# Performance work log

Measured on AMD Instinct MI355X. Metric: run time of the kernel, lower is better.

## Reference

```python
import jax, jax.numpy as jnp
import numpy as np

B, S, D, H = 8, 1024, 1024, 16
DK = D // H


def setup_inputs() -> dict:
    key = jax.random.key(0)
    ks = jax.random.split(key, 12)
    sc = 1.0 / np.sqrt(D)
    return {
        "query": jax.random.normal(ks[0], (B, S, D), jnp.float32),
        "key": jax.random.normal(ks[1], (B, S, D), jnp.float32),
        "value": jax.random.normal(ks[2], (B, S, D), jnp.float32),
        "Wq": jax.random.normal(ks[3], (D, D), jnp.float32) * sc,
        "bq": jnp.zeros((D,), jnp.float32),
        "Wk": jax.random.normal(ks[4], (D, D), jnp.float32) * sc,
        "bk": jnp.zeros((D,), jnp.float32),
        "Wv": jax.random.normal(ks[5], (D, D), jnp.float32) * sc,
        "bv": jnp.zeros((D,), jnp.float32),
        "Wa": jax.random.normal(ks[6], (D, D), jnp.float32) * sc,
        "ba": jnp.zeros((D,), jnp.float32),
        "qvec": jax.random.normal(ks[7], (D,), jnp.float32),
    }


def reference(query, key, value, Wq, bq, Wk, bk, Wv, bv, Wa, ba, qvec):
    # project and split heads: [B,S,D] -> [B,H,S,DK]
    def split(x, W, b):
        y = x @ W.T + b
        return y.reshape(B, S, H, DK).transpose(0, 2, 1, 3)

    q = split(query, Wq, bq)
    k = split(key, Wk, bk)
    v = split(value, Wv, bv)

    scores = jnp.einsum('bhqd,bhkd->bhqk', q, k) / jnp.sqrt(jnp.float32(DK))
    p = jax.nn.softmax(scores, axis=-1)          # dropout p=0 -> identity
    x = jnp.einsum('bhqk,bhkd->bhqd', p, v)
    x = x.transpose(0, 2, 1, 3).reshape(B, S, D)  # [B,S,D]

    # attention2 pooling head
    a = jnp.tanh(x @ Wa.T + ba) @ qvec           # [B,S]
    alpha = jax.nn.softmax(a, axis=-1)
    return jnp.einsum('bs,bsd->bd', alpha, x)    # [B,D]
```

## Files before the change

### kernel.cpp

```cpp
#include <hip/hip_runtime.h>

typedef __bf16 bf16;
typedef __attribute__((ext_vector_type(8))) __bf16 bf16x8;
typedef __attribute__((ext_vector_type(4))) __bf16 bf16x4;
typedef __attribute__((ext_vector_type(4))) float f32x4;

#define GLDS16(g, l) __builtin_amdgcn_global_load_lds( \
    (const __attribute__((address_space(1))) void*)(g), \
    (__attribute__((address_space(3))) void*)(l), 16, 0, 0)

#define MFMA16(a, b, c) __builtin_amdgcn_mfma_f32_16x16x32_bf16(a, b, c, 0, 0, 0)

#define TR16(dst, addr, off) \
  asm volatile("ds_read_b64_tr_b16 %0, %1 offset:" #off : "=v"(dst) : "v"(addr))

struct CvtAll { const float* in[7]; bf16* out[7]; };

__global__ __launch_bounds__(256) void f2b_all(CvtAll a) {
  const int i = blockIdx.x * 256 + threadIdx.x;
  const float* in;
  bf16* out;
  int off;
  if (blockIdx.y < 3) {
    in = a.in[blockIdx.y];
    out = a.out[blockIdx.y];
    off = i;
  } else {
    if (i >= 524288) return;
    const int widx = 3 + (i >> 17);
    in = a.in[widx];
    out = a.out[widx];
    off = i & 131071;
  }
  const f32x4* p = (const f32x4*)in + (size_t)off * 2;
  f32x4 x = p[0], y = p[1];
  bf16x8 o;
  o[0] = (bf16)x[0]; o[1] = (bf16)x[1]; o[2] = (bf16)x[2]; o[3] = (bf16)x[3];
  o[4] = (bf16)y[0]; o[5] = (bf16)y[1]; o[6] = (bf16)y[2]; o[7] = (bf16)y[3];
  ((bf16x8*)out)[off] = o;
}

template <int EPI, int MF>
__device__ __forceinline__ void gemm_body8(
    const bf16* __restrict__ A, const bf16* __restrict__ Bw,
    const float* __restrict__ bias, const float* __restrict__ qv,
    bf16* __restrict__ C, float* __restrict__ part,
    const int row0, const int col0, const int N, const int K) {
  constexpr int BM = MF * 32;
  constexpr int ASZ = MF * 1024;
  constexpr int BUF = 2 * ASZ + 16384;
  constexpr int RSH = (MF == 8) ? 8 : 7;
  __shared__ __attribute__((aligned(16))) bf16 L[2 * BUF];
  const int tid = threadIdx.x;
  const int wid = tid >> 6, lane = tid & 63;
  const int g = lane >> 4, lc = lane & 15;
  const int wr = wid >> 2, wc = wid & 3;

  const bf16* gA = A + (size_t)(row0 + (tid & (BM - 1))) * K + (tid >> RSH) * 8;
  const bf16* gB = Bw + (size_t)(col0 + (tid & 255)) * K + (tid >> 8) * 8;
  const int d0 = (tid - lane) * 8;

#define STG_A(T, kh) do { \
    const bf16* gp_ = gA + (T) * 64 + (kh) * 32; \
    bf16* lp_ = L + ((T) & 1) * BUF + (kh) * ASZ + d0; \
    GLDS16(gp_, lp_); \
    if constexpr (MF == 8) GLDS16(gp_ + 16, lp_ + 4096); } while (0)
#define STG_B(T, kh) do { \
    const bf16* gp_ = gB + (T) * 64 + (kh) * 32; \
    bf16* lp_ = L + ((T) & 1) * BUF + 2 * ASZ + (kh) * 8192 + d0; \
    GLDS16(gp_, lp_); GLDS16(gp_ + 16, lp_ + 4096); } while (0)
#define RD_A(c, kh) do { \
    _Pragma("unroll") for (int m_ = 0; m_ < MF; ++m_) \
      af[m_] = *(const bf16x8*)&L[(c) * BUF + (kh) * ASZ + g * (BM * 8) + \
                                  (wr * (MF * 16) + m_ * 16 + lc) * 8]; \
  } while (0)
#define RD_B(c, kh, nh) do { \
    bf[0] = *(const bf16x8*)&L[(c) * BUF + 2 * ASZ + (kh) * 8192 + g * 2048 + \
                               (wc * 64 + (nh) * 32 + lc) * 8]; \
    bf[1] = *(const bf16x8*)&L[(c) * BUF + 2 * ASZ + (kh) * 8192 + g * 2048 + \
                               (wc * 64 + (nh) * 32 + 16 + lc) * 8]; \
  } while (0)
#define BARS \
    __builtin_amdgcn_s_barrier(); \
    asm volatile("s_waitcnt lgkmcnt(0)" ::: "memory"); \
    __builtin_amdgcn_sched_barrier(0);
#define MM(nh) do { \
    __builtin_amdgcn_s_setprio(1); \
    _Pragma("unroll") for (int m_ = 0; m_ < MF; ++m_) { \
      acc[m_][(nh) * 2 + 0] = MFMA16(af[m_], bf[0], acc[m_][(nh) * 2 + 0]); \
      acc[m_][(nh) * 2 + 1] = MFMA16(af[m_], bf[1], acc[m_][(nh) * 2 + 1]); \
    } \
    __builtin_amdgcn_s_setprio(0); } while (0)
#define ENDP do { \
    __builtin_amdgcn_s_barrier(); \
    asm volatile("" ::: "memory"); \
    __builtin_amdgcn_sched_barrier(0); } while (0)
#define VGATE() do { \
    if constexpr (MF == 8) { asm volatile("s_waitcnt vmcnt(6)" ::: "memory"); } \
    else                   { asm volatile("s_waitcnt vmcnt(4)" ::: "memory"); } } while (0)

  const f32x4 z4 = {0.f, 0.f, 0.f, 0.f};
  f32x4 acc[MF][4];
#pragma unroll
  for (int m = 0; m < MF; ++m)
#pragma unroll
    for (int n = 0; n < 4; ++n) acc[m][n] = z4;

  bf16x8 af[MF], bf[2];
  const int NT = K >> 6;
  const int NI = NT >> 1;

  STG_A(0, 0); STG_B(0, 0); STG_A(0, 1); STG_B(0, 1);
  STG_A(1, 0); STG_B(1, 0); STG_A(1, 1);
  VGATE();
  ENDP;

  for (int i = 0; i < NI; ++i) {
    const int t1 = 2 * i + 1, t2 = 2 * i + 2, t3 = 2 * i + 3;
    const bool p2 = t2 < NT, p3 = t3 < NT;
    RD_A(0, 0); RD_B(0, 0, 0);
    STG_B(t1, 1);
    BARS; MM(0); ENDP;
    RD_B(0, 0, 1);
    if (p2) STG_A(t2, 0);
    BARS; MM(1); ENDP;
    RD_A(0, 1); RD_B(0, 1, 0);
    if (p2) STG_B(t2, 0);
    BARS; MM(0); ENDP;
    RD_B(0, 1, 1);
    if (p2) STG_A(t2, 1);
    BARS; MM(1);
    if (p2) { VGATE(); }
    else    { asm volatile("s_waitcnt vmcnt(0)" ::: "memory"); }
    ENDP;
    RD_A(1, 0); RD_B(1, 0, 0);
    if (p2) STG_B(t2, 1);
    BARS; MM(0); ENDP;
    RD_B(1, 0, 1);
    if (p3) STG_A(t3, 0);
    BARS; MM(1); ENDP;
    RD_A(1, 1); RD_B(1, 1, 0);
    if (p3) STG_B(t3, 0);
    BARS; MM(0); ENDP;
    RD_B(1, 1, 1);
    if (p3) STG_A(t3, 1);
    BARS; MM(1);
    VGATE();
    ENDP;
  }

#undef STG_A
#undef STG_B
#undef RD_A
#undef RD_B
#undef BARS
#undef MM
#undef ENDP
#undef VGATE

  if constexpr (EPI == 0) {
#pragma unroll
    for (int n = 0; n < 4; ++n) {
      const int col = col0 + wc * 64 + n * 16 + lc;
      const float bb = bias[col];
#pragma unroll
      for (int m = 0; m < MF; ++m)
#pragma unroll
        for (int r = 0; r < 4; ++r) {
          const int row = row0 + wr * (MF * 16) + m * 16 + g * 4 + r;
          C[(size_t)row * N + col] = (bf16)(acc[m][n][r] + bb);
        }
    }
  } else {
    float ps[MF][4];
#pragma unroll
    for (int m = 0; m < MF; ++m)
#pragma unroll
      for (int r = 0; r < 4; ++r) ps[m][r] = 0.f;
#pragma unroll
    for (int n = 0; n < 4; ++n) {
      const int col = col0 + wc * 64 + n * 16 + lc;
      const float bb = bias[col];
      const float qq = qv[col];
#pragma unroll
      for (int m = 0; m < MF; ++m)
#pragma unroll
        for (int r = 0; r < 4; ++r)
          ps[m][r] += tanhf(acc[m][n][r] + bb) * qq;
    }
    float* pdst = part + (size_t)((col0 >> 8) * 4 + wc) * 8192;
#pragma unroll
    for (int m = 0; m < MF; ++m)
#pragma unroll
      for (int r = 0; r < 4; ++r) {
        float v = ps[m][r];
        v += __shfl_xor(v, 1); v += __shfl_xor(v, 2);
        v += __shfl_xor(v, 4); v += __shfl_xor(v, 8);
        if (lc == 0) {
          const int row = row0 + wr * (MF * 16) + m * 16 + g * 4 + r;
          pdst[row] = v;
        }
      }
  }
}

__device__ __forceinline__ void swz128(int phys, int& row0, int& col0) {
  const int lg = (phys & 7) * 16 + (phys >> 3);
  row0 = (lg >> 2) * 256;
  col0 = (lg & 3) * 256;
}

__device__ __forceinline__ void swz256(int phys, int& row0, int& col0) {
  const int lg = (phys & 7) * 32 + (phys >> 3);
  row0 = (lg >> 2) * 128;
  col0 = (lg & 3) * 256;
}

struct GemmSet { const bf16* A; const bf16* Bw; const float* bias; bf16* C; };
struct Gemm3Args { GemmSet s[3]; };

__global__ __launch_bounds__(512, 2) void gemm3_kernel(Gemm3Args a) {
  const GemmSet s = a.s[blockIdx.y];
  int row0, col0;
  swz128(blockIdx.x, row0, col0);
  gemm_body8<0, 8>(s.A, s.Bw, s.bias, nullptr, s.C, nullptr, row0, col0, 1024, 1024);
}

__global__ __launch_bounds__(512, 2) void gemm_a_kernel(
    const bf16* __restrict__ A, const bf16* __restrict__ Bw,
    const float* __restrict__ bias, const float* __restrict__ qv,
    float* __restrict__ part) {
  int row0, col0;
  swz256(blockIdx.x, row0, col0);
  gemm_body8<1, 4>(A, Bw, bias, qv, nullptr, part, row0, col0, 1024, 1024);
}

__global__ __launch_bounds__(256) void attn_kernel(
    const bf16* __restrict__ qp, const bf16* __restrict__ kp,
    const bf16* __restrict__ vp, bf16* __restrict__ xb, float* __restrict__ xf) {
  constexpr int S = 1024, D = 1024;
  __shared__ __attribute__((aligned(16))) bf16 Ks[8192];
  __shared__ __attribute__((aligned(16))) bf16 Vs[8192];
  __shared__ __attribute__((aligned(16))) bf16 Ps[4096];
  const int tid = threadIdx.x, wid = tid >> 6, lane = tid & 63;
  const int g = lane >> 4, lc = lane & 15;
  const int b = blockIdx.x >> 4, h = blockIdx.x & 15;
  const int q0 = blockIdx.y * 64;
  const size_t base = (size_t)b * S * D + (size_t)h * 64;

  bf16x8 qf[2];
  {
    const bf16* qrow = qp + base + (size_t)(q0 + wid * 16 + lc) * D;
    qf[0] = *(const bf16x8*)(qrow + g * 8);
    qf[1] = *(const bf16x8*)(qrow + 32 + g * 8);
#pragma unroll
    for (int j = 0; j < 8; ++j) {
      qf[0][j] = (bf16)((float)qf[0][j] * 0.125f);
      qf[1][j] = (bf16)((float)qf[1][j] * 0.125f);
    }
  }
  float m_s = -1e30f, l_s = 0.f;
  const f32x4 z4 = {0.f, 0.f, 0.f, 0.f};
  f32x4 ax[4];
#pragma unroll
  for (int m = 0; m < 4; ++m) ax[m] = z4;

  const int c0 = tid, c1 = tid + 256;
  const bf16* gK0 = kp + base + (size_t)(c0 & 63) * D + (c0 >> 6) * 8;
  const bf16* gK1 = kp + base + (size_t)(c1 & 63) * D + (c1 >> 6) * 8;
  bf16* lK0 = Ks + (size_t)(c0 - lane) * 8;
  bf16* lK1 = Ks + (size_t)(c1 - lane) * 8;
  const bf16* gV0 = vp + base + (size_t)((c0 >> 5) * 4 + ((c0 >> 1) & 3)) * D +
                    ((c0 >> 3) & 3) * 16 + (c0 & 1) * 8;
  const bf16* gV1 = vp + base + (size_t)((c1 >> 5) * 4 + ((c1 >> 1) & 3)) * D +
                    ((c1 >> 3) & 3) * 16 + (c1 & 1) * 8;
  bf16* lV0 = Vs + (size_t)(c0 - lane) * 8;
  bf16* lV1 = Vs + (size_t)(c1 - lane) * 8;

  bf16* pw = Ps + wid * 1024;
  const int pswz_a = lc & 3, pswz_b = (lc >> 2) & 3;
  const unsigned vaddr0 =
      (unsigned)(uintptr_t)(const __attribute__((address_space(3))) bf16*)(Vs + 512 * g + 4 * lc);

  GLDS16(gK0, lK0);
  GLDS16(gK1, lK1);
  GLDS16(gV0, lV0);
  GLDS16(gV1, lV1);

  for (int t = 0; t < 16; ++t) {
    __syncthreads();
    const int cur = t & 1;
    if (t < 15) {
      const size_t off = (size_t)(t + 1) * 64 * D;
      const int nb = cur ^ 1;
      GLDS16(gK0 + off, lK0 + nb * 4096);
      GLDS16(gK1 + off, lK1 + nb * 4096);
      GLDS16(gV0 + off, lV0 + nb * 4096);
      GLDS16(gV1 + off, lV1 + nb * 4096);
    }
    const bf16* Kb = Ks + cur * 4096;
    const unsigned va = vaddr0 + cur * 8192u;

    f32x4 sc[4];
    __builtin_amdgcn_s_setprio(1);
#pragma unroll
    for (int m = 0; m < 4; ++m) {
      f32x4 z = z4;
      bf16x8 kf0 = *(const bf16x8*)(Kb + (size_t)g * 512 + (m * 16 + lc) * 8);
      bf16x8 kf1 = *(const bf16x8*)(Kb + (size_t)(4 + g) * 512 + (m * 16 + lc) * 8);
      z = MFMA16(kf0, qf[0], z);
      z = MFMA16(kf1, qf[1], z);
      sc[m] = z;
    }
    __builtin_amdgcn_s_setprio(0);

    float mx = -1e30f;
#pragma unroll
    for (int m = 0; m < 4; ++m)
      mx = fmaxf(mx, fmaxf(fmaxf(sc[m][0], sc[m][1]), fmaxf(sc[m][2], sc[m][3])));
    mx = fmaxf(mx, __shfl_xor(mx, 16));
    mx = fmaxf(mx, __shfl_xor(mx, 32));
    if (!__all(mx - m_s <= 8.f)) {
      const float mn = fmaxf(m_s, mx);
      const float cr = __expf(m_s - mn);
      l_s *= cr;
#pragma unroll
      for (int m = 0; m < 4; ++m) ax[m] *= cr;
      m_s = mn;
    }
    float sm = 0.f;
#pragma unroll
    for (int m = 0; m < 4; ++m)
#pragma unroll
      for (int r = 0; r < 4; ++r) {
        float p = __expf(sc[m][r] - m_s);
        sc[m][r] = p;
        sm += p;
      }
    sm += __shfl_xor(sm, 16);
    sm += __shfl_xor(sm, 32);
    l_s += sm;

#pragma unroll
    for (int m = 0; m < 4; ++m) {
      bf16x4 pk;
      pk[0] = (bf16)sc[m][0]; pk[1] = (bf16)sc[m][1];
      pk[2] = (bf16)sc[m][2]; pk[3] = (bf16)sc[m][3];
      *(bf16x4*)(pw + lc * 64 + 16 * (m ^ pswz_a) + 4 * (g ^ pswz_b)) = pk;
    }

    bf16x4 pr[2][2];
#pragma unroll
    for (int kk = 0; kk < 2; ++kk)
#pragma unroll
      for (int jh = 0; jh < 2; ++jh) {
        const int msrc = 2 * kk + (g >> 1);
        const int gsrc = (2 * g + jh) & 3;
        pr[kk][jh] = *(const bf16x4*)(pw + lc * 64 + 16 * (msrc ^ pswz_a) + 4 * (gsrc ^ pswz_b));
      }
    bf16x8 pf0 = __builtin_shufflevector(pr[0][0], pr[0][1], 0, 1, 2, 3, 4, 5, 6, 7);
    bf16x8 pf1 = __builtin_shufflevector(pr[1][0], pr[1][1], 0, 1, 2, 3, 4, 5, 6, 7);

    bf16x4 vt[4][2][2];
    TR16(vt[0][0][0], va, 0);    TR16(vt[1][0][0], va, 128);
    TR16(vt[2][0][0], va, 256);  TR16(vt[3][0][0], va, 384);
    TR16(vt[0][0][1], va, 512);  TR16(vt[1][0][1], va, 640);
    TR16(vt[2][0][1], va, 768);  TR16(vt[3][0][1], va, 896);
    TR16(vt[0][1][0], va, 4096); TR16(vt[1][1][0], va, 4224);
    TR16(vt[2][1][0], va, 4352); TR16(vt[3][1][0], va, 4480);
    TR16(vt[0][1][1], va, 4608); TR16(vt[1][1][1], va, 4736);
    TR16(vt[2][1][1], va, 4864); TR16(vt[3][1][1], va, 4992);
    asm volatile("s_waitcnt lgkmcnt(0)" ::: "memory");
    __builtin_amdgcn_sched_barrier(0);

    __builtin_amdgcn_s_setprio(1);
#pragma unroll
    for (int md = 0; md < 4; ++md) {
      bf16x8 a0 = __builtin_shufflevector(vt[md][0][0], vt[md][0][1], 0, 1, 2, 3, 4, 5, 6, 7);
      bf16x8 a1 = __builtin_shufflevector(vt[md][1][0], vt[md][1][1], 0, 1, 2, 3, 4, 5, 6, 7);
      ax[md] = MFMA16(a0, pf0, ax[md]);
      ax[md] = MFMA16(a1, pf1, ax[md]);
    }
    __builtin_amdgcn_s_setprio(0);
  }

  const float inv = 1.0f / l_s;
  const int qrow = q0 + wid * 16 + lc;
  float* xfr = xf + base + (size_t)qrow * D;
  bf16* xbr = xb + base + (size_t)qrow * D;
#pragma unroll
  for (int m = 0; m < 4; ++m) {
    f32x4 vv = ax[m] * inv;
    *(f32x4*)(xfr + 16 * m + 4 * g) = vv;
    bf16x4 bb;
    bb[0] = (bf16)vv[0]; bb[1] = (bf16)vv[1];
    bb[2] = (bf16)vv[2]; bb[3] = (bf16)vv[3];
    *(bf16x4*)(xbr + 16 * m + 4 * g) = bb;
  }
}

__global__ __launch_bounds__(256) void softmax_part(const float* __restrict__ part,
                                                    float* __restrict__ alpha) {
  __shared__ float red[8];
  const int b = blockIdx.x, t = threadIdx.x;
  f32x4 a4 = {0.f, 0.f, 0.f, 0.f};
#pragma unroll
  for (int p = 0; p < 16; ++p) {
    const float* pp = part + (size_t)p * 8192 + b * 1024 + t * 4;
    a4[0] += pp[0]; a4[1] += pp[1]; a4[2] += pp[2]; a4[3] += pp[3];
  }
  float m = fmaxf(fmaxf(a4[0], a4[1]), fmaxf(a4[2], a4[3]));
#pragma unroll
  for (int o = 1; o < 64; o <<= 1) m = fmaxf(m, __shfl_xor(m, o));
  if ((t & 63) == 0) red[t >> 6] = m;
  __syncthreads();
  m = fmaxf(fmaxf(red[0], red[1]), fmaxf(red[2], red[3]));
  f32x4 e;
  float s = 0.f;
#pragma unroll
  for (int j = 0; j < 4; ++j) { e[j] = __expf(a4[j] - m); s += e[j]; }
#pragma unroll
  for (int o = 1; o < 64; o <<= 1) s += __shfl_xor(s, o);
  if ((t & 63) == 0) red[4 + (t >> 6)] = s;
  __syncthreads();
  const float inv = 1.0f / (red[4] + red[5] + red[6] + red[7]);
  *(f32x4*)(alpha + b * 1024 + t * 4) = e * inv;
}

__global__ __launch_bounds__(256) void pool_kernel(const float* __restrict__ xf,
                                                   const float* __restrict__ alpha,
                                                   float* __restrict__ out) {
  const int b = blockIdx.y, sc = blockIdx.x, t = threadIdx.x;
  f32x4 acc = {0.f, 0.f, 0.f, 0.f};
  const float* xrow = xf + (size_t)b * 1024 * 1024;
  for (int s = sc * 64; s < sc * 64 + 64; ++s) {
    const float al = alpha[b * 1024 + s];
    f32x4 xv = *(const f32x4*)(xrow + (size_t)s * 1024 + t * 4);
    acc += xv * al;
  }
  atomicAdd(&out[b * 1024 + t * 4 + 0], acc[0]);
  atomicAdd(&out[b * 1024 + t * 4 + 1], acc[1]);
  atomicAdd(&out[b * 1024 + t * 4 + 2], acc[2]);
  atomicAdd(&out[b * 1024 + t * 4 + 3], acc[3]);
}

extern "C" void kernel_launch(void* const* d_in, const int* in_sizes, int n_in,
                              void* d_out, int out_size, void* d_ws, size_t ws_size,
                              hipStream_t stream) {
  const float* Q   = (const float*)d_in[0];
  const float* K   = (const float*)d_in[1];
  const float* V   = (const float*)d_in[2];
  const float* Wq  = (const float*)d_in[3];
  const float* bq  = (const float*)d_in[4];
  const float* Wk  = (const float*)d_in[5];
  const float* bk  = (const float*)d_in[6];
  const float* Wv  = (const float*)d_in[7];
  const float* bv  = (const float*)d_in[8];
  const float* Wa  = (const float*)d_in[9];
  const float* ba  = (const float*)d_in[10];
  const float* qvec = (const float*)d_in[11];
  float* out = (float*)d_out;
  char* ws = (char*)d_ws;
  const size_t MB = 1ull << 20;

  bf16* Wqb = (bf16*)(ws + 0 * MB);
  bf16* Wkb = (bf16*)(ws + 2 * MB);
  bf16* Wvb = (bf16*)(ws + 4 * MB);
  bf16* Wab = (bf16*)(ws + 6 * MB);
  bf16* qb  = (bf16*)(ws + 8 * MB);
  bf16* kb  = (bf16*)(ws + 24 * MB);
  bf16* vb  = (bf16*)(ws + 40 * MB);
  bf16* qp  = (bf16*)(ws + 56 * MB);
  bf16* kp  = (bf16*)(ws + 72 * MB);
  bf16* vp  = (bf16*)(ws + 88 * MB);
  float* part  = (float*)(ws + 104 * MB);
  float* alpha = (float*)(ws + 104 * MB + 524288);
  bf16* xb  = qb;
  float* xf = (float*)(ws + 24 * MB);

  hipMemsetAsync(out, 0, 8192 * sizeof(float), stream);

  CvtAll cv = {{Q, K, V, Wq, Wk, Wv, Wa}, {qb, kb, vb, Wqb, Wkb, Wvb, Wab}};
  f2b_all<<<dim3(4096, 4), 256, 0, stream>>>(cv);

  Gemm3Args g3 = {{{qb, Wqb, bq, qp}, {kb, Wkb, bk, kp}, {vb, Wvb, bv, vp}}};
  gemm3_kernel<<<dim3(128, 3), 512, 0, stream>>>(g3);

  attn_kernel<<<dim3(128, 16), 256, 0, stream>>>(qp, kp, vp, xb, xf);

  gemm_a_kernel<<<256, 512, 0, stream>>>(xb, Wab, ba, qvec, part);

  softmax_part<<<8, 256, 0, stream>>>(part, alpha);
  pool_kernel<<<dim3(16, 8), 256, 0, stream>>>(xf, alpha, out);
}
```

Measured before the change: 245.6 us.

## Process two 64-row query groups per attention block to reuse K/V tiles

```diff
diff --git a/kernel.cpp b/kernel.cpp
--- a/kernel.cpp
+++ b/kernel.cpp
@@ -241,29 +241,32 @@
   constexpr int S = 1024, D = 1024;
   __shared__ __attribute__((aligned(16))) bf16 Ks[8192];
   __shared__ __attribute__((aligned(16))) bf16 Vs[8192];
-  __shared__ __attribute__((aligned(16))) bf16 Ps[4096];
+  __shared__ __attribute__((aligned(16))) bf16 Ps[8192];
   const int tid = threadIdx.x, wid = tid >> 6, lane = tid & 63;
   const int g = lane >> 4, lc = lane & 15;
   const int b = blockIdx.x >> 4, h = blockIdx.x & 15;
-  const int q0 = blockIdx.y * 64;
+  const int q0 = blockIdx.y * 128;
   const size_t base = (size_t)b * S * D + (size_t)h * 64;
 
-  bf16x8 qf[2];
-  {
-    const bf16* qrow = qp + base + (size_t)(q0 + wid * 16 + lc) * D;
-    qf[0] = *(const bf16x8*)(qrow + g * 8);
-    qf[1] = *(const bf16x8*)(qrow + 32 + g * 8);
+  bf16x8 qf[2][2];
+#pragma unroll
+  for (int qg = 0; qg < 2; ++qg) {
+    const bf16* qrow = qp + base + (size_t)(q0 + qg * 64 + wid * 16 + lc) * D;
+    qf[qg][0] = *(const bf16x8*)(qrow + g * 8);
+    qf[qg][1] = *(const bf16x8*)(qrow + 32 + g * 8);
 #pragma unroll
     for (int j = 0; j < 8; ++j) {
-      qf[0][j] = (bf16)((float)qf[0][j] * 0.125f);
-      qf[1][j] = (bf16)((float)qf[1][j] * 0.125f);
+      qf[qg][0][j] = (bf16)((float)qf[qg][0][j] * 0.125f);
+      qf[qg][1][j] = (bf16)((float)qf[qg][1][j] * 0.125f);
     }
   }
-  float m_s = -1e30f, l_s = 0.f;
+  float m_s[2] = {-1e30f, -1e30f}, l_s[2] = {0.f, 0.f};
   const f32x4 z4 = {0.f, 0.f, 0.f, 0.f};
-  f32x4 ax[4];
-#pragma unroll
-  for (int m = 0; m < 4; ++m) ax[m] = z4;
+  f32x4 ax[2][4];
+#pragma unroll
+  for (int qg = 0; qg < 2; ++qg)
+#pragma unroll
+    for (int m = 0; m < 4; ++m) ax[qg][m] = z4;
 
   const int c0 = tid, c1 = tid + 256;
   const bf16* gK0 = kp + base + (size_t)(c0 & 63) * D + (c0 >> 6) * 8;
@@ -277,7 +280,7 @@
   bf16* lV0 = Vs + (size_t)(c0 - lane) * 8;
   bf16* lV1 = Vs + (size_t)(c1 - lane) * 8;
 
-  bf16* pw = Ps + wid * 1024;
+  bf16* pw = Ps + wid * 2048;
   const int pswz_a = lc & 3, pswz_b = (lc >> 2) & 3;
   const unsigned vaddr0 =
       (unsigned)(uintptr_t)(const __attribute__((address_space(3))) bf16*)(Vs + 512 * g + 4 * lc);
@@ -301,66 +304,6 @@
     const bf16* Kb = Ks + cur * 4096;
     const unsigned va = vaddr0 + cur * 8192u;
 
-    f32x4 sc[4];
-    __builtin_amdgcn_s_setprio(1);
-#pragma unroll
-    for (int m = 0; m < 4; ++m) {
-      f32x4 z = z4;
-      bf16x8 kf0 = *(const bf16x8*)(Kb + (size_t)g * 512 + (m * 16 + lc) * 8);
-      bf16x8 kf1 = *(const bf16x8*)(Kb + (size_t)(4 + g) * 512 + (m * 16 + lc) * 8);
-      z = MFMA16(kf0, qf[0], z);
-      z = MFMA16(kf1, qf[1], z);
-      sc[m] = z;
-    }
-    __builtin_amdgcn_s_setprio(0);
-
-    float mx = -1e30f;
-#pragma unroll
-    for (int m = 0; m < 4; ++m)
-      mx = fmaxf(mx, fmaxf(fmaxf(sc[m][0], sc[m][1]), fmaxf(sc[m][2], sc[m][3])));
-    mx = fmaxf(mx, __shfl_xor(mx, 16));
-    mx = fmaxf(mx, __shfl_xor(mx, 32));
-    if (!__all(mx - m_s <= 8.f)) {
-      const float mn = fmaxf(m_s, mx);
-      const float cr = __expf(m_s - mn);
-      l_s *= cr;
-#pragma unroll
-      for (int m = 0; m < 4; ++m) ax[m] *= cr;
-      m_s = mn;
-    }
-    float sm = 0.f;
-#pragma unroll
-    for (int m = 0; m < 4; ++m)
-#pragma unroll
-      for (int r = 0; r < 4; ++r) {
-        float p = __expf(sc[m][r] - m_s);
-        sc[m][r] = p;
-        sm += p;
-      }
-    sm += __shfl_xor(sm, 16);
-    sm += __shfl_xor(sm, 32);
-    l_s += sm;
-
-#pragma unroll
-    for (int m = 0; m < 4; ++m) {
-      bf16x4 pk;
-      pk[0] = (bf16)sc[m][0]; pk[1] = (bf16)sc[m][1];
-      pk[2] = (bf16)sc[m][2]; pk[3] = (bf16)sc[m][3];
-      *(bf16x4*)(pw + lc * 64 + 16 * (m ^ pswz_a) + 4 * (g ^ pswz_b)) = pk;
-    }
-
-    bf16x4 pr[2][2];
-#pragma unroll
-    for (int kk = 0; kk < 2; ++kk)
-#pragma unroll
-      for (int jh = 0; jh < 2; ++jh) {
-        const int msrc = 2 * kk + (g >> 1);
-        const int gsrc = (2 * g + jh) & 3;
-        pr[kk][jh] = *(const bf16x4*)(pw + lc * 64 + 16 * (msrc ^ pswz_a) + 4 * (gsrc ^ pswz_b));
-      }
-    bf16x8 pf0 = __builtin_shufflevector(pr[0][0], pr[0][1], 0, 1, 2, 3, 4, 5, 6, 7);
-    bf16x8 pf1 = __builtin_shufflevector(pr[1][0], pr[1][1], 0, 1, 2, 3, 4, 5, 6, 7);
-
     bf16x4 vt[4][2][2];
     TR16(vt[0][0][0], va, 0);    TR16(vt[1][0][0], va, 128);
     TR16(vt[2][0][0], va, 256);  TR16(vt[3][0][0], va, 384);
@@ -373,29 +316,96 @@
     asm volatile("s_waitcnt lgkmcnt(0)" ::: "memory");
     __builtin_amdgcn_sched_barrier(0);
 
-    __builtin_amdgcn_s_setprio(1);
-#pragma unroll
-    for (int md = 0; md < 4; ++md) {
-      bf16x8 a0 = __builtin_shufflevector(vt[md][0][0], vt[md][0][1], 0, 1, 2, 3, 4, 5, 6, 7);
-      bf16x8 a1 = __builtin_shufflevector(vt[md][1][0], vt[md][1][1], 0, 1, 2, 3, 4, 5, 6, 7);
-      ax[md] = MFMA16(a0, pf0, ax[md]);
-      ax[md] = MFMA16(a1, pf1, ax[md]);
+#pragma unroll
+    for (int qg = 0; qg < 2; ++qg) {
+      f32x4 sc[4];
+      __builtin_amdgcn_s_setprio(1);
+#pragma unroll
+      for (int m = 0; m < 4; ++m) {
+        f32x4 z = z4;
+        bf16x8 kf0 = *(const bf16x8*)(Kb + (size_t)g * 512 + (m * 16 + lc) * 8);
+        bf16x8 kf1 = *(const bf16x8*)(Kb + (size_t)(4 + g) * 512 + (m * 16 + lc) * 8);
+        z = MFMA16(kf0, qf[qg][0], z);
+        z = MFMA16(kf1, qf[qg][1], z);
+        sc[m] = z;
+      }
+      __builtin_amdgcn_s_setprio(0);
+
+      float mx = -1e30f;
+#pragma unroll
+      for (int m = 0; m < 4; ++m)
+        mx = fmaxf(mx, fmaxf(fmaxf(sc[m][0], sc[m][1]), fmaxf(sc[m][2], sc[m][3])));
+      mx = fmaxf(mx, __shfl_xor(mx, 16));
+      mx = fmaxf(mx, __shfl_xor(mx, 32));
+      if (!__all(mx - m_s[qg] <= 8.f)) {
+        const float mn = fmaxf(m_s[qg], mx);
+        const float cr = __expf(m_s[qg] - mn);
+        l_s[qg] *= cr;
+#pragma unroll
+        for (int m = 0; m < 4; ++m) ax[qg][m] *= cr;
+        m_s[qg] = mn;
+      }
+      float sm = 0.f;
+#pragma unroll
+      for (int m = 0; m < 4; ++m)
+#pragma unroll
+        for (int r = 0; r < 4; ++r) {
+          float p = __expf(sc[m][r] - m_s[qg]);
+          sc[m][r] = p;
+          sm += p;
+        }
+      sm += __shfl_xor(sm, 16);
+      sm += __shfl_xor(sm, 32);
+      l_s[qg] += sm;
+
+      bf16* pg = pw + qg * 1024;
+#pragma unroll
+      for (int m = 0; m < 4; ++m) {
+        bf16x4 pk;
+        pk[0] = (bf16)sc[m][0]; pk[1] = (bf16)sc[m][1];
+        pk[2] = (bf16)sc[m][2]; pk[3] = (bf16)sc[m][3];
+        *(bf16x4*)(pg + lc * 64 + 16 * (m ^ pswz_a) + 4 * (g ^ pswz_b)) = pk;
+      }
+
+      bf16x4 pr[2][2];
+#pragma unroll
+      for (int kk = 0; kk < 2; ++kk)
+#pragma unroll
+        for (int jh = 0; jh < 2; ++jh) {
+          const int msrc = 2 * kk + (g >> 1);
+          const int gsrc = (2 * g + jh) & 3;
+          pr[kk][jh] = *(const bf16x4*)(pg + lc * 64 + 16 * (msrc ^ pswz_a) + 4 * (gsrc ^ pswz_b));
+        }
+      bf16x8 pf0 = __builtin_shufflevector(pr[0][0], pr[0][1], 0, 1, 2, 3, 4, 5, 6, 7);
+      bf16x8 pf1 = __builtin_shufflevector(pr[1][0], pr[1][1], 0, 1, 2, 3, 4, 5, 6, 7);
+
+      __builtin_amdgcn_s_setprio(1);
+#pragma unroll
+      for (int md = 0; md < 4; ++md) {
+        bf16x8 a0 = __builtin_shufflevector(vt[md][0][0], vt[md][0][1], 0, 1, 2, 3, 4, 5, 6, 7);
+        bf16x8 a1 = __builtin_shufflevector(vt[md][1][0], vt[md][1][1], 0, 1, 2, 3, 4, 5, 6, 7);
+        ax[qg][md] = MFMA16(a0, pf0, ax[qg][md]);
+        ax[qg][md] = MFMA16(a1, pf1, ax[qg][md]);
+      }
+      __builtin_amdgcn_s_setprio(0);
     }
-    __builtin_amdgcn_s_setprio(0);
-  }
-
-  const float inv = 1.0f / l_s;
-  const int qrow = q0 + wid * 16 + lc;
-  float* xfr = xf + base + (size_t)qrow * D;
-  bf16* xbr = xb + base + (size_t)qrow * D;
-#pragma unroll
-  for (int m = 0; m < 4; ++m) {
-    f32x4 vv = ax[m] * inv;
-    *(f32x4*)(xfr + 16 * m + 4 * g) = vv;
-    bf16x4 bb;
-    bb[0] = (bf16)vv[0]; bb[1] = (bf16)vv[1];
-    bb[2] = (bf16)vv[2]; bb[3] = (bf16)vv[3];
-    *(bf16x4*)(xbr + 16 * m + 4 * g) = bb;
+  }
+
+#pragma unroll
+  for (int qg = 0; qg < 2; ++qg) {
+    const float inv = 1.0f / l_s[qg];
+    const int qrow = q0 + qg * 64 + wid * 16 + lc;
+    float* xfr = xf + base + (size_t)qrow * D;
+    bf16* xbr = xb + base + (size_t)qrow * D;
+#pragma unroll
+    for (int m = 0; m < 4; ++m) {
+      f32x4 vv = ax[qg][m] * inv;
+      *(f32x4*)(xfr + 16 * m + 4 * g) = vv;
+      bf16x4 bb;
+      bb[0] = (bf16)vv[0]; bb[1] = (bf16)vv[1];
+      bb[2] = (bf16)vv[2]; bb[3] = (bf16)vv[3];
+      *(bf16x4*)(xbr + 16 * m + 4 * g) = bb;
+    }
   }
 }
 
@@ -486,7 +496,7 @@
   Gemm3Args g3 = {{{qb, Wqb, bq, qp}, {kb, Wkb, bk, kp}, {vb, Wvb, bv, vp}}};
   gemm3_kernel<<<dim3(128, 3), 512, 0, stream>>>(g3);
 
-  attn_kernel<<<dim3(128, 16), 256, 0, stream>>>(qp, kp, vp, xb, xf);
+  attn_kernel<<<dim3(128, 8), 256, 0, stream>>>(qp, kp, vp, xb, xf);
 
   gemm_a_kernel<<<256, 512, 0, stream>>>(xb, Wab, ba, qvec, part);
 
```

Measured after the change: 246.2 us. About the same (+0.2%).
